# Performance work log

Measured on AMD Instinct MI355X. Metric: run time of the kernel, lower is better.

Reference implementation:

```python
import jax, jax.numpy as jnp
import numpy as np

BANDWIDTH = 1.0


def setup_inputs() -> dict:
    key = jax.random.key(0)
    k1, k2 = jax.random.split(key)
    test_Xs = jax.random.normal(k1, (4096, 16), dtype=jnp.float32)
    train_Xs = jax.random.normal(k2, (8192, 16), dtype=jnp.float32)
    return {"test_Xs": test_Xs, "train_Xs": train_Xs}


def reference(test_Xs, train_Xs):
    n, d = train_Xs.shape
    h = jnp.float32(BANDWIDTH)
    # log normalization constant of n Gaussian kernels with bandwidth h in d dims
    Z = 0.5 * d * jnp.log(2 * jnp.float32(np.pi)) + d * jnp.log(h) + jnp.log(jnp.float32(n))
    # diffs: [n_test, n_train, d]
    diffs = (test_Xs[:, None, :] - train_Xs[None, :, :]) / h
    log_exp = -0.5 * jnp.sum(diffs * diffs, axis=-1)  # [n_test, n_train]
    return jax.scipy.special.logsumexp(log_exp - Z, axis=-1)  # [n_test]
```

## Files before the change

kernel.cpp:

```cpp
#include <hip/hip_runtime.h>
#include <math.h>

#define LOG2E 1.4426950408889634f
#define LN2   0.6931471805599453f
#define NW 16
#define CH 64

typedef short short8 __attribute__((ext_vector_type(8)));
typedef float f32x16 __attribute__((ext_vector_type(16)));

__device__ inline unsigned int cvtpk_bf16(float lo, float hi) {
    unsigned int r;
    asm("v_cvt_pk_bf16_f32 %0, %1, %2" : "=v"(r) : "v"(lo), "v"(hi));
    return r;
}

__global__ __launch_bounds__(1024, 4) void kde_fused(
    const float* __restrict__ testX, const float* __restrict__ trainX,
    float* __restrict__ out, int nTest, int nTrain, int nch, float Z)
{
    const int tid  = threadIdx.x;
    const int lane = tid & 63;
    const int w    = tid >> 6;
    const int c    = lane & 31;
    const int half = lane >> 5;
    const int rowBase = blockIdx.x * 16;

    __shared__ short8 stage[NW][2 * CH];
    __shared__ float  wbuf[NW][CH];
    __shared__ float  xnbuf[16];
    __shared__ __align__(16) float red2[NW][32][20];
    __shared__ float  red3[16][68];

    const int mrow = min(rowBase + (c & 15), nTest - 1);
    const float4* xp = (const float4*)(testX + (size_t)mrow * 16) + half * 2;
    float4 xa = xp[0], xb = xp[1];
    float f0 = xa.x*LOG2E, f1 = xa.y*LOG2E, f2 = xa.z*LOG2E, f3 = xa.w*LOG2E;
    float f4 = xb.x*LOG2E, f5 = xb.y*LOG2E, f6 = xb.z*LOG2E, f7 = xb.w*LOG2E;
    float pn = ((f0*f0 + f1*f1) + (f2*f2 + f3*f3))
             + ((f4*f4 + f5*f5) + (f6*f6 + f7*f7));
    float xn2 = (pn + __shfl_xor(pn, 32)) * (0.5f / LOG2E);
    union { unsigned int u[4]; short8 s; } au;
    au.u[0] = cvtpk_bf16(f0, f1);
    au.u[1] = cvtpk_bf16(f2, f3);
    au.u[2] = cvtpk_bf16(f4, f5);
    au.u[3] = cvtpk_bf16(f6, f7);
    const short8 afrag = au.s;
    if (w == 0 && half == 0 && c < 16) xnbuf[c] = xn2;

    const int nMax = nTrain - 1;
    const int tb   = w * nch * CH;
    const int rdU  = (c * 2 + half) ^ ((c >> 2) & 7);

    float4 q0, q1, q2, q3; float wv;
    auto LOADRAW = [&](int ch) {
        int gi = tb + ch * CH + lane;
        const float4* p = (const float4*)(trainX + (size_t)min(gi, nMax) * 16);
        q0 = p[0]; q1 = p[1]; q2 = p[2]; q3 = p[3];
        float nrm = ((q0.x*q0.x + q0.y*q0.y) + (q0.z*q0.z + q0.w*q0.w))
                  + ((q1.x*q1.x + q1.y*q1.y) + (q1.z*q1.z + q1.w*q1.w))
                  + ((q2.x*q2.x + q2.y*q2.y) + (q2.z*q2.z + q2.w*q2.w))
                  + ((q3.x*q3.x + q3.y*q3.y) + (q3.z*q3.z + q3.w*q3.w));
        wv = (gi <= nMax) ? __builtin_amdgcn_exp2f(-0.5f * LOG2E * nrm) : 0.0f;
    };
    auto WRITEPT = [&]() {
        const int pp = lane & 31, ti = lane >> 5;
        const int u0 = (pp * 2 + 0) ^ ((pp >> 2) & 7);
        const int u1 = (pp * 2 + 1) ^ ((pp >> 2) & 7);
        union { unsigned int u[4]; short8 s; } b0, b1;
        b0.u[0] = cvtpk_bf16(q0.x, q0.y); b0.u[1] = cvtpk_bf16(q0.z, q0.w);
        b0.u[2] = cvtpk_bf16(q1.x, q1.y); b0.u[3] = cvtpk_bf16(q1.z, q1.w);
        b1.u[0] = cvtpk_bf16(q2.x, q2.y); b1.u[1] = cvtpk_bf16(q2.z, q2.w);
        b1.u[2] = cvtpk_bf16(q3.x, q3.y); b1.u[3] = cvtpk_bf16(q3.z, q3.w);
        stage[w][ti * 64 + u0] = b0.s;
        stage[w][ti * 64 + u1] = b1.s;
        wbuf[w][lane] = wv;
    };

    float rs[8];
    #pragma unroll
    for (int i = 0; i < 8; ++i) rs[i] = 0.0f;

    const f32x16 zc = {0.f,0.f,0.f,0.f,0.f,0.f,0.f,0.f,
                       0.f,0.f,0.f,0.f,0.f,0.f,0.f,0.f};
    auto INNER = [&]() {
        short8 bf0 = stage[w][rdU];
        short8 bf1 = stage[w][64 + rdU];
        float  wt0 = wbuf[w][c];
        float  wt1 = wbuf[w][32 + c];
        f32x16 d0 = __builtin_amdgcn_mfma_f32_32x32x16_bf16(afrag, bf0, zc, 0,0,0);
        f32x16 d1 = __builtin_amdgcn_mfma_f32_32x32x16_bf16(afrag, bf1, zc, 0,0,0);
        #pragma unroll
        for (int r = 0; r < 8; ++r)
            rs[r] += __builtin_amdgcn_exp2f(d0[r]) * wt0;
        #pragma unroll
        for (int r = 0; r < 8; ++r)
            rs[r] += __builtin_amdgcn_exp2f(d1[r]) * wt1;
    };

    LOADRAW(0);
    WRITEPT();
    for (int ch = 0; ch < nch - 1; ++ch) {
        LOADRAW(ch + 1);
        INNER();
        WRITEPT();
    }
    INNER();

    {
        float4 v0 = make_float4(rs[0], rs[1], rs[2], rs[3]);
        float4 v1 = make_float4(rs[4], rs[5], rs[6], rs[7]);
        *(float4*)&red2[w][c][half * 4]     = v0;
        *(float4*)&red2[w][c][8 + half * 4] = v1;
    }
    __syncthreads();

    {
        int row = tid & 15, seg = tid >> 4;
        int wv2 = seg >> 2, cb = (seg & 3) * 8;
        float s = 0.0f;
        #pragma unroll
        for (int i = 0; i < 8; ++i) s += red2[wv2][cb + i][row];
        red3[row][seg] = s;
    }
    __syncthreads();

    if (tid < 16) {
        int row = rowBase + tid;
        if (row < nTest) {
            float s = 0.0f;
            #pragma unroll
            for (int k = 0; k < 64; ++k) s += red3[tid][k];
            out[row] = __logf(s) - xnbuf[tid] * LN2 - Z;
        }
    }
}

extern "C" void kernel_launch(void* const* d_in, const int* in_sizes, int n_in,
                              void* d_out, int out_size, void* d_ws, size_t ws_size,
                              hipStream_t stream) {
    const float* testX  = (const float*)d_in[0];
    const float* trainX = (const float*)d_in[1];
    float* out = (float*)d_out;

    const int D = 16;
    const int nTest  = in_sizes[0] / D;
    const int nTrain = in_sizes[1] / D;

    const float Z = 0.5f * (float)D * logf(2.0f * (float)M_PI) + logf((float)nTrain);

    const int nch  = (nTrain + NW * CH - 1) / (NW * CH);
    const int grid = (nTest + 15) / 16;

    kde_fused<<<grid, 1024, 0, stream>>>(testX, trainX, out, nTest, nTrain, nch, Z);
}
```

Measured before the change: 14.95 us.

## Double-buffer per-wave LDS staging and prefetch train points two chunks ahead

Per-wave LDS staging buffers for train points are doubled. The loop is unrolled by two so global loads for chunk ch+2 are issued while the MFMA/exp work of chunk ch runs, and the norm/exp2 weight computation moves from load time to write time so loads stay independent. The chunk count is rounded up to an even number, which adds masked padding work for odd counts. The final reduction now reads red3 with float4 loads. The cost is more registers and shared memory per block, which may reduce occupancy.

After: 15.80 us. +5.7%, slower.

```diff
diff --git a/kernel.cpp b/kernel.cpp
--- a/kernel.cpp
+++ b/kernel.cpp
@@ -26,11 +26,11 @@
     const int half = lane >> 5;
     const int rowBase = blockIdx.x * 16;
 
-    __shared__ short8 stage[NW][2 * CH];
-    __shared__ float  wbuf[NW][CH];
+    __shared__ short8 stage[NW][2][2 * CH];
+    __shared__ float  wbuf[NW][2][CH];
     __shared__ float  xnbuf[16];
     __shared__ __align__(16) float red2[NW][32][20];
-    __shared__ float  red3[16][68];
+    __shared__ __align__(16) float red3[16][68];
 
     const int mrow = min(rowBase + (c & 15), nTest - 1);
     const float4* xp = (const float4*)(testX + (size_t)mrow * 16) + half * 2;
@@ -51,61 +51,72 @@
     const int nMax = nTrain - 1;
     const int tb   = w * nch * CH;
     const int rdU  = (c * 2 + half) ^ ((c >> 2) & 7);
-
-    float4 q0, q1, q2, q3; float wv;
-    auto LOADRAW = [&](int ch) {
-        int gi = tb + ch * CH + lane;
-        const float4* p = (const float4*)(trainX + (size_t)min(gi, nMax) * 16);
-        q0 = p[0]; q1 = p[1]; q2 = p[2]; q3 = p[3];
-        float nrm = ((q0.x*q0.x + q0.y*q0.y) + (q0.z*q0.z + q0.w*q0.w))
-                  + ((q1.x*q1.x + q1.y*q1.y) + (q1.z*q1.z + q1.w*q1.w))
-                  + ((q2.x*q2.x + q2.y*q2.y) + (q2.z*q2.z + q2.w*q2.w))
-                  + ((q3.x*q3.x + q3.y*q3.y) + (q3.z*q3.z + q3.w*q3.w));
-        wv = (gi <= nMax) ? __builtin_amdgcn_exp2f(-0.5f * LOG2E * nrm) : 0.0f;
-    };
-    auto WRITEPT = [&]() {
-        const int pp = lane & 31, ti = lane >> 5;
-        const int u0 = (pp * 2 + 0) ^ ((pp >> 2) & 7);
-        const int u1 = (pp * 2 + 1) ^ ((pp >> 2) & 7);
-        union { unsigned int u[4]; short8 s; } b0, b1;
-        b0.u[0] = cvtpk_bf16(q0.x, q0.y); b0.u[1] = cvtpk_bf16(q0.z, q0.w);
-        b0.u[2] = cvtpk_bf16(q1.x, q1.y); b0.u[3] = cvtpk_bf16(q1.z, q1.w);
-        b1.u[0] = cvtpk_bf16(q2.x, q2.y); b1.u[1] = cvtpk_bf16(q2.z, q2.w);
-        b1.u[2] = cvtpk_bf16(q3.x, q3.y); b1.u[3] = cvtpk_bf16(q3.z, q3.w);
-        stage[w][ti * 64 + u0] = b0.s;
-        stage[w][ti * 64 + u1] = b1.s;
-        wbuf[w][lane] = wv;
-    };
+    const int pp   = lane & 31, ti64 = lane >> 5;
+    const int u0s  = (pp * 2 + 0) ^ ((pp >> 2) & 7);
+    const int u1s  = (pp * 2 + 1) ^ ((pp >> 2) & 7);
 
     float rs[8];
     #pragma unroll
     for (int i = 0; i < 8; ++i) rs[i] = 0.0f;
-
     const f32x16 zc = {0.f,0.f,0.f,0.f,0.f,0.f,0.f,0.f,
                        0.f,0.f,0.f,0.f,0.f,0.f,0.f,0.f};
-    auto INNER = [&]() {
-        short8 bf0 = stage[w][rdU];
-        short8 bf1 = stage[w][64 + rdU];
-        float  wt0 = wbuf[w][c];
-        float  wt1 = wbuf[w][32 + c];
-        f32x16 d0 = __builtin_amdgcn_mfma_f32_32x32x16_bf16(afrag, bf0, zc, 0,0,0);
-        f32x16 d1 = __builtin_amdgcn_mfma_f32_32x32x16_bf16(afrag, bf1, zc, 0,0,0);
-        #pragma unroll
-        for (int r = 0; r < 8; ++r)
-            rs[r] += __builtin_amdgcn_exp2f(d0[r]) * wt0;
-        #pragma unroll
-        for (int r = 0; r < 8; ++r)
-            rs[r] += __builtin_amdgcn_exp2f(d1[r]) * wt1;
-    };
 
-    LOADRAW(0);
-    WRITEPT();
-    for (int ch = 0; ch < nch - 1; ++ch) {
-        LOADRAW(ch + 1);
-        INNER();
-        WRITEPT();
+    #define LOADPT(CHN, Q0,Q1,Q2,Q3,VLD) {                                    \
+        int gi = tb + (CHN) * CH + lane;                                      \
+        VLD = (gi <= nMax);                                                   \
+        const float4* p = (const float4*)(trainX + (size_t)min(gi, nMax)*16); \
+        Q0 = p[0]; Q1 = p[1]; Q2 = p[2]; Q3 = p[3]; }
+
+    #define WRITEPT(Q0,Q1,Q2,Q3,VLD,B) {                                      \
+        float nrm = ((Q0.x*Q0.x + Q0.y*Q0.y) + (Q0.z*Q0.z + Q0.w*Q0.w))       \
+                  + ((Q1.x*Q1.x + Q1.y*Q1.y) + (Q1.z*Q1.z + Q1.w*Q1.w))       \
+                  + ((Q2.x*Q2.x + Q2.y*Q2.y) + (Q2.z*Q2.z + Q2.w*Q2.w))       \
+                  + ((Q3.x*Q3.x + Q3.y*Q3.y) + (Q3.z*Q3.z + Q3.w*Q3.w));      \
+        float wvv = (VLD) ? __builtin_amdgcn_exp2f(-0.5f*LOG2E*nrm) : 0.0f;   \
+        union { unsigned int u[4]; short8 s; } bu0, bu1;                      \
+        bu0.u[0]=cvtpk_bf16(Q0.x,Q0.y); bu0.u[1]=cvtpk_bf16(Q0.z,Q0.w);       \
+        bu0.u[2]=cvtpk_bf16(Q1.x,Q1.y); bu0.u[3]=cvtpk_bf16(Q1.z,Q1.w);       \
+        bu1.u[0]=cvtpk_bf16(Q2.x,Q2.y); bu1.u[1]=cvtpk_bf16(Q2.z,Q2.w);       \
+        bu1.u[2]=cvtpk_bf16(Q3.x,Q3.y); bu1.u[3]=cvtpk_bf16(Q3.z,Q3.w);       \
+        stage[w][B][ti64 * 64 + u0s] = bu0.s;                                 \
+        stage[w][B][ti64 * 64 + u1s] = bu1.s;                                 \
+        wbuf[w][B][lane] = wvv; }
+
+    #define INNER(B) {                                                        \
+        short8 bf0 = stage[w][B][rdU];                                        \
+        short8 bf1 = stage[w][B][64 + rdU];                                   \
+        float  wt0 = wbuf[w][B][c];                                           \
+        float  wt1 = wbuf[w][B][32 + c];                                      \
+        f32x16 d0 = __builtin_amdgcn_mfma_f32_32x32x16_bf16(afrag,bf0,zc,0,0,0);\
+        f32x16 d1 = __builtin_amdgcn_mfma_f32_32x32x16_bf16(afrag,bf1,zc,0,0,0);\
+        _Pragma("unroll")                                                     \
+        for (int r = 0; r < 8; ++r)                                           \
+            rs[r] += __builtin_amdgcn_exp2f(d0[r]) * wt0;                     \
+        _Pragma("unroll")                                                     \
+        for (int r = 0; r < 8; ++r)                                           \
+            rs[r] += __builtin_amdgcn_exp2f(d1[r]) * wt1; }
+
+    float4 ra0,ra1,ra2,ra3, rb0,rb1,rb2,rb3;
+    bool vA, vB;
+    LOADPT(0, ra0,ra1,ra2,ra3, vA);
+    LOADPT(1, rb0,rb1,rb2,rb3, vB);
+    WRITEPT(ra0,ra1,ra2,ra3, vA, 0);
+    int ch = 0;
+    for (; ch + 2 < nch; ch += 2) {
+        INNER(0);
+        LOADPT(ch + 2, ra0,ra1,ra2,ra3, vA);
+        WRITEPT(rb0,rb1,rb2,rb3, vB, 1);
+        INNER(1);
+        LOADPT(ch + 3, rb0,rb1,rb2,rb3, vB);
+        WRITEPT(ra0,ra1,ra2,ra3, vA, 0);
     }
-    INNER();
+    INNER(0);
+    WRITEPT(rb0,rb1,rb2,rb3, vB, 1);
+    INNER(1);
+
+    #undef LOADPT
+    #undef WRITEPT
+    #undef INNER
 
     {
         float4 v0 = make_float4(rs[0], rs[1], rs[2], rs[3]);
@@ -130,7 +141,10 @@
         if (row < nTest) {
             float s = 0.0f;
             #pragma unroll
-            for (int k = 0; k < 64; ++k) s += red3[tid][k];
+            for (int k = 0; k < 16; ++k) {
+                float4 v = *(const float4*)&red3[tid][k * 4];
+                s += (v.x + v.y) + (v.z + v.w);
+            }
             out[row] = __logf(s) - xnbuf[tid] * LN2 - Z;
         }
     }
@@ -149,7 +163,8 @@
 
     const float Z = 0.5f * (float)D * logf(2.0f * (float)M_PI) + logf((float)nTrain);
 
-    const int nch  = (nTrain + NW * CH - 1) / (NW * CH);
+    int nch = (nTrain + NW * CH - 1) / (NW * CH);
+    nch = (nch + 1) & ~1;
     const int grid = (nTest + 15) / 16;
 
     kde_fused<<<grid, 1024, 0, stream>>>(testX, trainX, out, nTest, nTrain, nch, Z);
```
